# Optimization experiments

Measured on AMD Instinct MI355X. Metric: run time of the kernel, lower is better.

Reference implementation:

```python
import jax, jax.numpy as jnp
import numpy as np

EMBED_DIM = 1024
HEADS = 16
D_K = EMBED_DIM // HEADS
B, S = 2, 2048


def setup_inputs() -> dict:
    key = jax.random.key(0)
    ks = jax.random.split(key, 8)
    scale = 1.0 / np.sqrt(EMBED_DIM)
    inp = {
        "key": jax.random.normal(ks[0], (B, S, EMBED_DIM), dtype=jnp.float32),
        "query": jax.random.normal(ks[1], (B, S, EMBED_DIM), dtype=jnp.float32),
        "value": jax.random.normal(ks[2], (B, S, EMBED_DIM), dtype=jnp.float32),
        # torch nn.Linear stores weight as [out, in]; y = x @ W.T
        "Wq": jax.random.normal(ks[3], (EMBED_DIM, EMBED_DIM), dtype=jnp.float32) * scale,
        "Wk": jax.random.normal(ks[4], (EMBED_DIM, EMBED_DIM), dtype=jnp.float32) * scale,
        "Wv": jax.random.normal(ks[5], (EMBED_DIM, EMBED_DIM), dtype=jnp.float32) * scale,
        "Wo": jax.random.normal(ks[6], (EMBED_DIM, EMBED_DIM), dtype=jnp.float32) * scale,
        "bo": jax.random.normal(ks[7], (EMBED_DIM,), dtype=jnp.float32) * scale,
        # causal mask, True = keep (matches masked_fill(~mask, -1e20))
        "mask": jnp.tril(jnp.ones((S, S), dtype=jnp.bool_))[None, None, :, :],
    }
    return inp


def _split_heads(x):
    b, s, _ = x.shape
    return x.reshape(b, s, HEADS, D_K).transpose(0, 2, 1, 3)  # [B,H,S,d_k]


def reference(key, query, value, Wq, Wk, Wv, Wo, bo, mask):
    b, q_len = query.shape[0], query.shape[1]
    k = _split_heads(key @ Wk.T)
    q = _split_heads(query @ Wq.T)
    v = _split_heads(value @ Wv.T)
    scores = jnp.einsum('bhqd,bhkd->bhqk', q, k) / np.sqrt(D_K)
    scores = jnp.where(mask, scores, jnp.float32(-1e20))
    attn = jax.nn.softmax(scores, axis=-1)
    out = jnp.einsum('bhqk,bhkd->bhqd', attn, v)
    out = out.transpose(0, 2, 1, 3).reshape(b, q_len, HEADS * D_K)
    return out @ Wo.T + bo
```

## Files before the change

### kernel.cpp

```cpp
#include <hip/hip_runtime.h>
#include <cstdint>
#include <cstddef>


typedef __bf16 bf16;
typedef __bf16 bf16x4 __attribute__((ext_vector_type(4)));
typedef __bf16 bf16x8 __attribute__((ext_vector_type(8)));
typedef float f32x4 __attribute__((ext_vector_type(4)));

#define MFMA(a, b, c) __builtin_amdgcn_mfma_f32_16x16x32_bf16(a, b, c, 0, 0, 0)

constexpr int EMBED = 1024;
constexpr int SEQ = 2048;
constexpr int HEADS = 16;
constexpr int DK = 64;
constexpr int BH = 32;

__device__ __forceinline__ void gl16(const bf16* g, bf16* l) {
  __builtin_amdgcn_global_load_lds(
      (const __attribute__((address_space(1))) unsigned int*)g,
      (__attribute__((address_space(3))) unsigned int*)l, 16, 0, 0);
}

__global__ __launch_bounds__(256) void probe_kernel(const unsigned short* __restrict__ wq,
                                                    int* __restrict__ flag) {
  __shared__ int cnt;
  int t = threadIdx.x;
  if (t == 0) cnt = 0;
  __syncthreads();
  unsigned short u = wq[2 * t];
  int e = (u >> 7) & 0xFF;
  int sane = (e >= 100 && e <= 130) ? 1 : 0;
  atomicAdd(&cnt, sane);
  __syncthreads();
  if (t == 0) flag[0] = (cnt < 128) ? 1 : 0;
}

struct ConvArgs {
  const void* src[8];
  bf16* dst[8];
  int n8[8];
  const int* flag;
};

__global__ __launch_bounds__(256) void convert_kernel(ConvArgs a) {
  const int seg = blockIdx.y;
  const void* s = a.src[seg];
  bf16* d = a.dst[seg];
  const int n8 = a.n8[seg];
  const int isf32 = a.flag[0];
  for (int i = blockIdx.x * 256 + threadIdx.x; i < n8; i += gridDim.x * 256) {
    if (isf32) {
      const float* sp = (const float*)s + (size_t)i * 8;
      float4 x = *(const float4*)sp, y = *(const float4*)(sp + 4);
      bf16x8 v;
      v[0] = (bf16)x.x; v[1] = (bf16)x.y; v[2] = (bf16)x.z; v[3] = (bf16)x.w;
      v[4] = (bf16)y.x; v[5] = (bf16)y.y; v[6] = (bf16)y.z; v[7] = (bf16)y.w;
      *(bf16x8*)(d + (size_t)i * 8) = v;
    } else {
      *(uint4*)(d + (size_t)i * 8) = *(const uint4*)((const bf16*)s + (size_t)i * 8);
    }
  }
}

__device__ __forceinline__ void gemm_body(
    const bf16* __restrict__ X, const bf16* __restrict__ W,
    const bf16* __restrict__ bias, bf16* __restrict__ outb,
    float* __restrict__ outf, int mode, bf16* As, bf16* Bs, int m0, int n0)
{
  const int t = threadIdx.x;
  const int lane = t & 63, wave = t >> 6;
  const int wm = wave >> 1, wn = wave & 1;
  const int l16 = lane & 15, quad = lane >> 4;

  f32x4 acc[4][2] = {};

  for (int k0 = 0; k0 < EMBED; k0 += 64) {
    __syncthreads();
#pragma unroll
    for (int i = 0; i < 4; ++i) {
      int idx = t + i * 256;
      int r = idx >> 3;
      int cl = (idx & 7) ^ (r & 7);
      gl16(X + (size_t)(m0 + r) * EMBED + k0 + cl * 8, As + (wave * 64 + i * 256) * 8);
    }
#pragma unroll
    for (int i = 0; i < 2; ++i) {
      int idx = t + i * 256;
      int r = idx >> 3;
      int cl = (idx & 7) ^ (r & 7);
      gl16(W + (size_t)(n0 + r) * EMBED + k0 + cl * 8, Bs + (wave * 64 + i * 256) * 8);
    }
    __syncthreads();

#pragma unroll
    for (int ks = 0; ks < 2; ++ks) {
      bf16x8 a[4], b[2];
#pragma unroll
      for (int mi = 0; mi < 4; ++mi) {
        int row = wm * 64 + mi * 16 + l16;
        a[mi] = *(const bf16x8*)(As + row * 64 + (((ks * 4 + quad) ^ (row & 7)) * 8));
      }
#pragma unroll
      for (int ni = 0; ni < 2; ++ni) {
        int row = wn * 32 + ni * 16 + l16;
        b[ni] = *(const bf16x8*)(Bs + row * 64 + (((ks * 4 + quad) ^ (row & 7)) * 8));
      }
#pragma unroll
      for (int mi = 0; mi < 4; ++mi)
#pragma unroll
        for (int ni = 0; ni < 2; ++ni)
          acc[mi][ni] = MFMA(a[mi], b[ni], acc[mi][ni]);
    }
  }

#pragma unroll
  for (int mi = 0; mi < 4; ++mi) {
#pragma unroll
    for (int ni = 0; ni < 2; ++ni) {
      int n = n0 + wn * 32 + ni * 16 + l16;
#pragma unroll
      for (int r = 0; r < 4; ++r) {
        int m = m0 + wm * 64 + mi * 16 + quad * 4 + r;
        float v = acc[mi][ni][r];
        if (mode == 2) {
          outf[(size_t)m * EMBED + n] = v + (float)bias[n];
        } else {
          int b_ = m >> 11, s = m & (SEQ - 1);
          int h = n >> 6, d = n & 63;
          int bh = b_ * HEADS + h;
          if (mode == 0)
            outb[((size_t)bh * SEQ + s) * DK + d] = (bf16)v;
          else
            outb[((size_t)bh * DK + d) * SEQ + s] = (bf16)v;
        }
      }
    }
  }
}

struct QkvArgs {
  const bf16 *X0, *X1, *X2;
  const bf16 *W0, *W1, *W2;
  bf16 *O0, *O1, *O2;
};

__global__ __launch_bounds__(256) void qkv_gemm(QkvArgs args) {
  __shared__ alignas(16) bf16 As[128 * 64];
  __shared__ alignas(16) bf16 Bs[64 * 64];
  const int z = blockIdx.z;
  const bf16* X = (z == 0) ? args.X0 : (z == 1) ? args.X1 : args.X2;
  const bf16* W = (z == 0) ? args.W0 : (z == 1) ? args.W1 : args.W2;
  bf16* O      = (z == 0) ? args.O0 : (z == 1) ? args.O1 : args.O2;
  int mode = (z == 2) ? 1 : 0;
  gemm_body(X, W, nullptr, O, nullptr, mode, As, Bs,
            blockIdx.x * 128, blockIdx.y * 64);
}

__global__ __launch_bounds__(256) void out_gemm(const bf16* __restrict__ X,
                                               const bf16* __restrict__ W,
                                               const bf16* __restrict__ bias,
                                               float* __restrict__ out) {
  __shared__ alignas(16) bf16 As[128 * 64];
  __shared__ alignas(16) bf16 Bs[64 * 64];
  gemm_body(X, W, bias, nullptr, out, 2, As, Bs,
            blockIdx.x * 128, blockIdx.y * 64);
}

__global__ __launch_bounds__(512, 4) void attn_kernel(
    const bf16* __restrict__ qbuf, const bf16* __restrict__ kbuf,
    const bf16* __restrict__ vtbuf, bf16* __restrict__ ctx)
{
  __shared__ alignas(16) bf16 Qs[128 * 64];
  __shared__ alignas(16) bf16 Ks[64 * 64];
  __shared__ alignas(16) bf16 VTs[64 * 64];
  __shared__ alignas(16) bf16 Ps[128 * 72];

  const int t = threadIdx.x;
  const int g = (blockIdx.x + blockIdx.y) & 15;
  const int qt = (blockIdx.y & 16) ? (15 - g) : g;
  const int bh = blockIdx.y;
  const int q0 = qt * 128;
  const int lane = t & 63, w = t >> 6;
  const int l16 = lane & 15, quad = lane >> 4;

  const bf16* Qg = qbuf + ((size_t)bh * SEQ + q0) * DK;
#pragma unroll
  for (int i = 0; i < 2; ++i) {
    int idx = t + i * 512;
    int r = idx >> 3;
    int cl = (idx & 7) ^ (r & 7);
    gl16(Qg + (size_t)r * DK + cl * 8, Qs + (w * 64 + i * 512) * 8);
  }
  __syncthreads();

  bf16x8 qf[2];
  {
    int row = w * 16 + l16;
#pragma unroll
    for (int ks = 0; ks < 2; ++ks)
      qf[ks] = *(const bf16x8*)(Qs + row * 64 + (((ks * 4 + quad) ^ (row & 7)) * 8));
  }

  const int qglob = q0 + w * 16 + l16;
  float lst = 0.f;
  f32x4 o[4] = {};
  bf16* Pw = Ps + w * 16 * 72;

  constexpr float SC = 0.125f * 1.44269504f;
  constexpr float BI = -8.0f * 1.44269504f;

  const int ktmax = 2 * qt + 1;
  for (int kt = 0; kt <= ktmax; ++kt) {
    __syncthreads();
    const bf16* Kg = kbuf + ((size_t)bh * SEQ + kt * 64) * DK;
    const bf16* Vg = vtbuf + (size_t)bh * DK * SEQ + kt * 64;
    {
      int r = t >> 3;
      int cl = (t & 7) ^ (r & 7);
      gl16(Kg + (size_t)r * DK + cl * 8, Ks + w * 512);
      gl16(Vg + (size_t)r * SEQ + cl * 8, VTs + w * 512);
    }
    __syncthreads();

    f32x4 sacc[4] = {};
#pragma unroll
    for (int ks = 0; ks < 2; ++ks) {
#pragma unroll
      for (int mi = 0; mi < 4; ++mi) {
        int row = mi * 16 + l16;
        bf16x8 kf = *(const bf16x8*)(Ks + row * 64 + (((ks * 4 + quad) ^ (row & 7)) * 8));
        sacc[mi] = MFMA(kf, qf[ks], sacc[mi]);
      }
    }

    const bool need_mask = (kt * 64 + 63 > q0 + w * 16);
    float ls = 0.f;
    const int kbase = kt * 64 + quad * 4;
#pragma unroll
    for (int mi = 0; mi < 4; ++mi) {
      bf16x4 pv;
#pragma unroll
      for (int r = 0; r < 4; ++r) {
        float arg = __builtin_fmaf(sacc[mi][r], SC, BI);
        if (need_mask && (kbase + mi * 16 + r > qglob)) arg = -1e30f;
        float p = __builtin_exp2f(arg);
        ls += p;
        pv[r] = (bf16)p;
      }
      *(bf16x4*)(Pw + l16 * 72 + mi * 16 + quad * 4) = pv;
    }
    ls += __shfl_xor(ls, 16);
    ls += __shfl_xor(ls, 32);
    lst += ls;

#pragma unroll
    for (int ks = 0; ks < 2; ++ks) {
      bf16x8 pf = *(const bf16x8*)(Pw + l16 * 72 + ks * 32 + quad * 8);
#pragma unroll
      for (int dt = 0; dt < 4; ++dt) {
        bf16x8 vf = *(const bf16x8*)(VTs + (dt * 16 + l16) * 64 +
                                     (((ks * 4 + quad) ^ ((dt * 16 + l16) & 7)) * 8));
        o[dt] = MFMA(vf, pf, o[dt]);
      }
    }
  }

  const float inv = 1.0f / lst;
  const int b_ = bh >> 4, h = bh & 15;
  bf16* dst = ctx + ((size_t)b_ * SEQ + qglob) * EMBED + h * DK;
#pragma unroll
  for (int dt = 0; dt < 4; ++dt) {
    bf16x4 v;
#pragma unroll
    for (int r = 0; r < 4; ++r) v[r] = (bf16)(o[dt][r] * inv);
    *(bf16x4*)(dst + dt * 16 + quad * 4) = v;
  }
}

extern "C" void kernel_launch(void* const* d_in, const int* in_sizes, int n_in,
                              void* d_out, int out_size, void* d_ws, size_t ws_size,
                              hipStream_t stream) {
  const void* key   = d_in[0];
  const void* query = d_in[1];
  const void* value = d_in[2];
  const void* Wq    = d_in[3];
  const void* Wk    = d_in[4];
  const void* Wv    = d_in[5];
  const void* Wo    = d_in[6];
  const void* bo    = d_in[7];
  float* out = (float*)d_out;

  int* flag = (int*)d_ws;
  char* base = (char*)d_ws + 256;
  const size_t XN = (size_t)2 * SEQ * EMBED;
  const size_t WN = (size_t)EMBED * EMBED;
  const size_t per = (size_t)BH * SEQ * DK;

  bf16* cq  = (bf16*)base;
  bf16* ck  = cq + XN;
  bf16* cv  = ck + XN;
  bf16* cWq = cv + XN;
  bf16* cWk = cWq + WN;
  bf16* cWv = cWk + WN;
  bf16* cWo = cWv + WN;
  bf16* cbo = cWo + WN;
  bf16* qb  = cbo + 1024;
  bf16* kb  = qb + per;
  bf16* vtb = kb + per;
  bf16* ctx = vtb + per;

  probe_kernel<<<1, 256, 0, stream>>>((const unsigned short*)Wq, flag);

  ConvArgs ca;
  ca.src[0] = query; ca.dst[0] = cq;  ca.n8[0] = (int)(XN / 8);
  ca.src[1] = key;   ca.dst[1] = ck;  ca.n8[1] = (int)(XN / 8);
  ca.src[2] = value; ca.dst[2] = cv;  ca.n8[2] = (int)(XN / 8);
  ca.src[3] = Wq;    ca.dst[3] = cWq; ca.n8[3] = (int)(WN / 8);
  ca.src[4] = Wk;    ca.dst[4] = cWk; ca.n8[4] = (int)(WN / 8);
  ca.src[5] = Wv;    ca.dst[5] = cWv; ca.n8[5] = (int)(WN / 8);
  ca.src[6] = Wo;    ca.dst[6] = cWo; ca.n8[6] = (int)(WN / 8);
  ca.src[7] = bo;    ca.dst[7] = cbo; ca.n8[7] = 128;
  ca.flag = flag;
  convert_kernel<<<dim3(2048, 8), 256, 0, stream>>>(ca);

  QkvArgs qa{cq, ck, cv, cWq, cWk, cWv, qb, kb, vtb};
  qkv_gemm<<<dim3(32, 16, 3), 256, 0, stream>>>(qa);
  attn_kernel<<<dim3(16, 32), 512, 0, stream>>>(qb, kb, vtb, ctx);
  out_gemm<<<dim3(32, 16), 256, 0, stream>>>(ctx, cWo, cbo, out);
}
```

Before: 240.1 us.

## Load Q, K and V fragments directly from global memory in attention kernel

```diff
diff --git a/kernel.cpp b/kernel.cpp
--- a/kernel.cpp
+++ b/kernel.cpp
@@ -171,9 +171,6 @@
     const bf16* __restrict__ qbuf, const bf16* __restrict__ kbuf,
     const bf16* __restrict__ vtbuf, bf16* __restrict__ ctx)
 {
-  __shared__ alignas(16) bf16 Qs[128 * 64];
-  __shared__ alignas(16) bf16 Ks[64 * 64];
-  __shared__ alignas(16) bf16 VTs[64 * 64];
   __shared__ alignas(16) bf16 Ps[128 * 72];
 
   const int t = threadIdx.x;
@@ -184,23 +181,10 @@
   const int lane = t & 63, w = t >> 6;
   const int l16 = lane & 15, quad = lane >> 4;
 
-  const bf16* Qg = qbuf + ((size_t)bh * SEQ + q0) * DK;
-#pragma unroll
-  for (int i = 0; i < 2; ++i) {
-    int idx = t + i * 512;
-    int r = idx >> 3;
-    int cl = (idx & 7) ^ (r & 7);
-    gl16(Qg + (size_t)r * DK + cl * 8, Qs + (w * 64 + i * 512) * 8);
-  }
-  __syncthreads();
-
+  const bf16* Qg = qbuf + ((size_t)bh * SEQ + q0 + w * 16 + l16) * DK;
   bf16x8 qf[2];
-  {
-    int row = w * 16 + l16;
-#pragma unroll
-    for (int ks = 0; ks < 2; ++ks)
-      qf[ks] = *(const bf16x8*)(Qs + row * 64 + (((ks * 4 + quad) ^ (row & 7)) * 8));
-  }
+  qf[0] = *(const bf16x8*)(Qg + quad * 8);
+  qf[1] = *(const bf16x8*)(Qg + 32 + quad * 8);
 
   const int qglob = q0 + w * 16 + l16;
   float lst = 0.f;
@@ -210,26 +194,21 @@
   constexpr float SC = 0.125f * 1.44269504f;
   constexpr float BI = -8.0f * 1.44269504f;
 
+  const bf16* Kp0 = kbuf + (size_t)bh * SEQ * DK;
+  const bf16* Vp0 = vtbuf + (size_t)bh * DK * SEQ;
+
   const int ktmax = 2 * qt + 1;
   for (int kt = 0; kt <= ktmax; ++kt) {
-    __syncthreads();
-    const bf16* Kg = kbuf + ((size_t)bh * SEQ + kt * 64) * DK;
-    const bf16* Vg = vtbuf + (size_t)bh * DK * SEQ + kt * 64;
-    {
-      int r = t >> 3;
-      int cl = (t & 7) ^ (r & 7);
-      gl16(Kg + (size_t)r * DK + cl * 8, Ks + w * 512);
-      gl16(Vg + (size_t)r * SEQ + cl * 8, VTs + w * 512);
-    }
-    __syncthreads();
+    const bf16* Kp = Kp0 + (size_t)kt * 64 * DK;
+    const bf16* Vp = Vp0 + kt * 64;
 
     f32x4 sacc[4] = {};
 #pragma unroll
     for (int ks = 0; ks < 2; ++ks) {
 #pragma unroll
       for (int mi = 0; mi < 4; ++mi) {
-        int row = mi * 16 + l16;
-        bf16x8 kf = *(const bf16x8*)(Ks + row * 64 + (((ks * 4 + quad) ^ (row & 7)) * 8));
+        bf16x8 kf = *(const bf16x8*)(Kp + (size_t)(mi * 16 + l16) * DK +
+                                     ks * 32 + quad * 8);
         sacc[mi] = MFMA(kf, qf[ks], sacc[mi]);
       }
     }
@@ -259,8 +238,8 @@
       bf16x8 pf = *(const bf16x8*)(Pw + l16 * 72 + ks * 32 + quad * 8);
 #pragma unroll
       for (int dt = 0; dt < 4; ++dt) {
-        bf16x8 vf = *(const bf16x8*)(VTs + (dt * 16 + l16) * 64 +
-                                     (((ks * 4 + quad) ^ ((dt * 16 + l16) & 7)) * 8));
+        bf16x8 vf = *(const bf16x8*)(Vp + (size_t)(dt * 16 + l16) * SEQ +
+                                     ks * 32 + quad * 8);
         o[dt] = MFMA(vf, pf, o[dt]);
       }
     }
```

New measurement: 303.1 us. +26.2%, slower.
